# Performance work log

Hardware: AMD Instinct MI355X
Metric: run time of the kernel (lower is better)

The kernel has to match this reference:

```python
import jax, jax.numpy as jnp
import numpy as np

B, I, J, C = 1, 256, 256, 128
H, D = 4, 32          # no_heads, head_dim; c_hidden = H*D = 128
INF = 1.0e9
LN_EPS = 1e-5


def setup_inputs() -> dict:
    key = jax.random.key(0)
    ks = jax.random.split(key, 8)
    x = jax.random.normal(ks[0], (B, I, J, C), dtype=jnp.float32)
    mask = (jax.random.uniform(ks[1], (B, I, J)) > 0.1).astype(jnp.float32)
    std = 0.02
    wq = std * jax.random.normal(ks[2], (H * D, C), dtype=jnp.float32)
    wk = std * jax.random.normal(ks[3], (H * D, C), dtype=jnp.float32)
    wv = std * jax.random.normal(ks[4], (H * D, C), dtype=jnp.float32)
    wb = std * jax.random.normal(ks[5], (H, C), dtype=jnp.float32)
    wo = (std / np.sqrt(2 * H)) * jax.random.normal(ks[6], (C, H * D), dtype=jnp.float32)
    wo_b = jnp.zeros((C,), dtype=jnp.float32)
    ln_g = jnp.ones((C,), dtype=jnp.float32)
    ln_b = jnp.zeros((C,), dtype=jnp.float32)
    return {"x": x, "mask": mask, "ln_g": ln_g, "ln_b": ln_b,
            "wq": wq, "wk": wk, "wv": wv, "wb": wb, "wo": wo, "wo_b": wo_b}


def reference(x, mask, ln_g, ln_b, wq, wk, wv, wb, wo, wo_b):
    # LayerNorm over channel dim
    mu = jnp.mean(x, axis=-1, keepdims=True)
    var = jnp.mean(jnp.square(x - mu), axis=-1, keepdims=True)
    xn = (x - mu) * jax.lax.rsqrt(var + LN_EPS) * ln_g + ln_b

    # QKV projections (torch Linear: y = x @ W^T), reshape to heads
    q = (xn @ wq.T).reshape(B, I, J, H, D)
    k = (xn @ wk.T).reshape(B, I, J, H, D)
    v = (xn @ wv.T).reshape(B, I, J, H, D)

    scale = 1.0 / np.sqrt(D)
    # attention within each row i over the J dimension: [B, I, H, Jq, Jk]
    scores = jnp.einsum('biqhd,bikhd->bihqk', q, k) * scale

    # triangle bias: [B, I, J, H] -> [B, I, H, Jq, 1], broadcast over keys
    tb = jnp.einsum('bijc,hc->bijh', xn, wb)
    scores = scores + jnp.swapaxes(tb, -1, -2)[..., None]

    # mask bias: inf*(mask-1) -> [B, I, 1, Jq, 1] (as in the torch code)
    scores = scores + (INF * (mask - 1.0))[:, :, None, :, None]

    attn = jax.nn.softmax(scores, axis=-1)
    out = jnp.einsum('bihqk,bikhd->biqhd', attn, v).reshape(B, I, J, H * D)
    return out @ wo.T + wo_b
```

## Files before the change

kernel.cpp:

```cpp
#include <hip/hip_runtime.h>
#include <hip/hip_bf16.h>

typedef short bf16x8 __attribute__((ext_vector_type(8)));
typedef short bf16x4 __attribute__((ext_vector_type(4)));
typedef float f32x4  __attribute__((ext_vector_type(4)));

#define NI 256
#define NJ 256
#define NC 128
#define NH 4
#define ND 32

#define WB_OFF    0
#define WO_BF_OFF 98304
#define QG_OFF    131072
#define KG_OFF    16908288
#define VTG_OFF   37879808
#define TBM_OFF   55181312
#define OG_OFF    56229888

__device__ __forceinline__ short f2bf(float f) {
    return __builtin_bit_cast(short, __float2bfloat16(f));
}

typedef __attribute__((address_space(1))) const void gvoid_t;
typedef __attribute__((address_space(3))) void svoid_t;
__device__ __forceinline__ void load_lds16(const void* g, void* l) {
    __builtin_amdgcn_global_load_lds((gvoid_t*)g, (svoid_t*)l, 16, 0, 0);
}

__global__ __launch_bounds__(256, 8)
void k_conv(const float* __restrict__ wq, const float* __restrict__ wk,
            const float* __restrict__ wv, const float* __restrict__ wo,
            char* __restrict__ ws)
{
    const int gt = blockIdx.x * 256 + threadIdx.x;
    const int base = gt * 4;
    const float* src;
    short* dst;
    if (base < 49152) {
        const int t = base >> 14;
        src = (t == 0 ? wq : (t == 1 ? wk : wv)) + (base & 16383);
        dst = (short*)(ws + WB_OFF) + base;
    } else {
        src = wo + (base - 49152);
        dst = (short*)(ws + WO_BF_OFF) + (base - 49152);
    }
    f32x4 v = *(const f32x4*)src;
    bf16x4 o;
    #pragma unroll
    for (int r = 0; r < 4; ++r) o[r] = f2bf(v[r]);
    *(bf16x4*)dst = o;
}

__global__ __launch_bounds__(512, 4)
void k_pre(const float* __restrict__ x, const float* __restrict__ mask,
           const float* __restrict__ ln_g, const float* __restrict__ ln_b,
           const float* __restrict__ wb, char* __restrict__ ws)
{
    __shared__ char xn_s[128 * 256];

    const int tid  = threadIdx.x;
    const int lane = tid & 63;
    const int wid  = tid >> 6;
    const int g    = lane >> 4;
    const int l16  = lane & 15;
    const int b    = blockIdx.x;
    const int i    = b >> 1;
    const int half = b & 1;
    const int j0   = half * 128;

    {
        const int t  = tid >> 2;
        const int p  = tid & 3;
        const int ch = p * 32;
        const float* xr = x + ((size_t)(i * NJ) + j0 + t) * NC + ch;
        f32x4 vx[8];
        float s0 = 0.f;
        #pragma unroll
        for (int u = 0; u < 8; ++u) {
            vx[u] = *(const f32x4*)(xr + 4 * u);
            s0 += vx[u][0] + vx[u][1] + vx[u][2] + vx[u][3];
        }
        s0 += __shfl_xor(s0, 1);
        s0 += __shfl_xor(s0, 2);
        const float mu = s0 * 0.0078125f;
        float v0 = 0.f;
        #pragma unroll
        for (int u = 0; u < 8; ++u) {
            #pragma unroll
            for (int e = 0; e < 4; ++e) { float d = vx[u][e] - mu; v0 += d * d; }
        }
        v0 += __shfl_xor(v0, 1);
        v0 += __shfl_xor(v0, 2);
        const float rs = rsqrtf(v0 * 0.0078125f + 1e-5f);
        #pragma unroll
        for (int u = 0; u < 8; ++u) {
            f32x4 gg = *(const f32x4*)(ln_g + ch + 4 * u);
            f32x4 bb = *(const f32x4*)(ln_b + ch + 4 * u);
            #pragma unroll
            for (int e = 0; e < 4; ++e) vx[u][e] = (vx[u][e] - mu) * rs * gg[e] + bb[e];
        }
        float tb[4];
        #pragma unroll
        for (int h = 0; h < 4; ++h) {
            const float* wr = wb + h * NC + ch;
            float a = 0.f;
            #pragma unroll
            for (int u = 0; u < 8; ++u) {
                f32x4 w4 = *(const f32x4*)(wr + 4 * u);
                #pragma unroll
                for (int e = 0; e < 4; ++e) a += vx[u][e] * w4[e];
            }
            a += __shfl_xor(a, 1);
            a += __shfl_xor(a, 2);
            tb[h] = a;
        }
        if (p == 0) {
            const float mb = 1.0e9f * (mask[(size_t)i * NJ + j0 + t] - 1.0f);
            float* tbm = (float*)(ws + TBM_OFF);
            #pragma unroll
            for (int h = 0; h < 4; ++h)
                tbm[((size_t)(i * NH) + h) * NJ + j0 + t] = tb[h] + mb;
        }
        #pragma unroll
        for (int cc = 0; cc < 4; ++cc) {
            bf16x8 o8;
            #pragma unroll
            for (int e = 0; e < 4; ++e) {
                o8[e]     = f2bf(vx[2 * cc][e]);
                o8[4 + e] = f2bf(vx[2 * cc + 1][e]);
            }
            const int chunk = (p * 4 + cc) ^ (t & 7);
            *(bf16x8*)(xn_s + t * 256 + chunk * 16) = o8;
        }
    }
    __syncthreads();

    const f32x4 z4 = {0.f, 0.f, 0.f, 0.f};
    bf16x8 bfr[3][4];
    #pragma unroll
    for (int s = 0; s < 3; ++s) {
        const int n0 = wid * 48 + s * 16;
        const short* wr = (const short*)(ws + WB_OFF) + (size_t)(n0 + l16) * NC + g * 8;
        #pragma unroll
        for (int ks = 0; ks < 4; ++ks) bfr[s][ks] = *(const bf16x8*)(wr + ks * 32);
    }

    for (int mt = 0; mt < 8; ++mt) {
        const int row = mt * 16 + l16;
        bf16x8 af[4];
        #pragma unroll
        for (int ks = 0; ks < 4; ++ks) {
            const int chunk = (ks * 4 + g) ^ (row & 7);
            af[ks] = *(const bf16x8*)(xn_s + row * 256 + chunk * 16);
        }
        #pragma unroll
        for (int s = 0; s < 3; ++s) {
            f32x4 acc = z4;
            #pragma unroll
            for (int ks = 0; ks < 4; ++ks)
                acc = __builtin_amdgcn_mfma_f32_16x16x32_bf16(af[ks], bfr[s][ks], acc, 0, 0, 0);

            const int gr  = wid * 48 + s * 16;
            const int buf = gr >> 7;
            const int h   = (gr >> 5) & 3;
            const int dd0 = gr & 31;
            const size_t ih = (size_t)(i * NH) + h;
            const int tok = j0 + mt * 16 + g * 4;
            if (buf == 0) {
                short* qg = (short*)(ws + QG_OFF) + ih * 8192;
                #pragma unroll
                for (int r = 0; r < 4; ++r) qg[(tok + r) * 32 + dd0 + l16] = f2bf(acc[r]);
            } else if (buf == 1) {
                short* kg = (short*)(ws + KG_OFF) + ih * 10240;
                #pragma unroll
                for (int r = 0; r < 4; ++r) kg[(tok + r) * 40 + dd0 + l16] = f2bf(acc[r]);
            } else {
                short* vt = (short*)(ws + VTG_OFF) + ih * 8448;
                bf16x4 pk;
                #pragma unroll
                for (int r = 0; r < 4; ++r) pk[r] = f2bf(acc[r]);
                *(bf16x4*)(vt + (size_t)(dd0 + l16) * 264 + tok) = pk;
            }
        }
    }
}

__global__ __launch_bounds__(512, 4)
void k_attn(char* __restrict__ ws)
{
    __shared__ short kls[256][40];
    __shared__ char  vls[17408];
    __shared__ short pbuf[8][2][16][40];

    const int tid  = threadIdx.x;
    const int lane = tid & 63;
    const int wid  = tid >> 6;
    const int g    = lane >> 4;
    const int l16  = lane & 15;
    const size_t ih = blockIdx.x;
    const int i = (int)(ih >> 2);
    const int h = (int)(ih & 3);

    const short* qg  = (const short*)(ws + QG_OFF) + ih * 8192;
    const char*  kgp = ws + KG_OFF + ih * 20480;
    const char*  vtp = ws + VTG_OFF + ih * 16896;
    const float* tbm = (const float*)(ws + TBM_OFF) + ih * NJ;
    short* og = (short*)(ws + OG_OFF);

    for (int c = wid; c < 37; c += 8) {
        if (c < 20)      load_lds16(kgp + c * 1024 + lane * 16, (char*)kls + c * 1024);
        else if (c < 36) load_lds16(vtp + (c - 20) * 1024 + lane * 16, vls + (c - 20) * 1024);
        else if (lane < 32) load_lds16(vtp + 16384 + lane * 16, vls + 16384);
    }
    __syncthreads();

    const float SCALE = 0.17677669529663687f;
    const f32x4 z4 = {0.f, 0.f, 0.f, 0.f};

    #pragma unroll
    for (int qt = 0; qt < 2; ++qt) {
        const int tq = wid * 32 + qt * 16;
        f32x4 tbmb = *(const f32x4*)(tbm + tq + g * 4);

        bf16x8 qf = *(const bf16x8*)(qg + (size_t)(tq + l16) * 32 + g * 8);
        f32x4 s[16];
        #pragma unroll
        for (int kt = 0; kt < 16; ++kt) {
            bf16x8 kf = *(const bf16x8*)(&kls[kt * 16 + l16][g * 8]);
            s[kt] = __builtin_amdgcn_mfma_f32_16x16x32_bf16(qf, kf, z4, 0, 0, 0);
        }
        #pragma unroll
        for (int kt = 0; kt < 16; ++kt)
            #pragma unroll
            for (int r = 0; r < 4; ++r)
                s[kt][r] = fmaf(s[kt][r], SCALE, tbmb[r]);

        f32x4 mx = s[0];
        #pragma unroll
        for (int kt = 1; kt < 16; ++kt)
            #pragma unroll
            for (int r = 0; r < 4; ++r) mx[r] = fmaxf(mx[r], s[kt][r]);
        #pragma unroll
        for (int d = 1; d < 16; d <<= 1)
            #pragma unroll
            for (int r = 0; r < 4; ++r) mx[r] = fmaxf(mx[r], __shfl_xor(mx[r], d));

        f32x4 sum = z4;
        #pragma unroll
        for (int kt = 0; kt < 16; ++kt)
            #pragma unroll
            for (int r = 0; r < 4; ++r) { s[kt][r] = __expf(s[kt][r] - mx[r]); sum[r] += s[kt][r]; }
        #pragma unroll
        for (int d = 1; d < 16; d <<= 1)
            #pragma unroll
            for (int r = 0; r < 4; ++r) sum[r] += __shfl_xor(sum[r], d);
        f32x4 inv;
        #pragma unroll
        for (int r = 0; r < 4; ++r) inv[r] = 1.0f / sum[r];
        #pragma unroll
        for (int kt = 0; kt < 16; ++kt)
            #pragma unroll
            for (int r = 0; r < 4; ++r) s[kt][r] *= inv[r];

        f32x4 oacc0 = z4, oacc1 = z4;
        #pragma unroll
        for (int c = 0; c < 8; ++c) {
            short* pb = &pbuf[wid][c & 1][0][0];
            #pragma unroll
            for (int kk = 0; kk < 2; ++kk) {
                #pragma unroll
                for (int r = 0; r < 4; ++r)
                    pb[(g * 4 + r) * 40 + kk * 16 + l16] = f2bf(s[c * 2 + kk][r]);
            }
            bf16x8 a   = *(const bf16x8*)(pb + l16 * 40 + g * 8);
            bf16x8 vb0 = *(const bf16x8*)((const short*)(vls + (size_t)l16 * 528) + c * 32 + g * 8);
            bf16x8 vb1 = *(const bf16x8*)((const short*)(vls + (size_t)(16 + l16) * 528) + c * 32 + g * 8);
            oacc0 = __builtin_amdgcn_mfma_f32_16x16x32_bf16(a, vb0, oacc0, 0, 0, 0);
            oacc1 = __builtin_amdgcn_mfma_f32_16x16x32_bf16(a, vb1, oacc1, 0, 0, 0);
        }

        #pragma unroll
        for (int r = 0; r < 4; ++r) {
            const size_t row = (size_t)(i * NJ) + tq + g * 4 + r;
            og[row * 136 + h * 32 + l16]      = f2bf(oacc0[r]);
            og[row * 136 + h * 32 + 16 + l16] = f2bf(oacc1[r]);
        }
    }
}

__global__ __launch_bounds__(512, 4)
void k_oproj(const char* __restrict__ ws, const float* __restrict__ wo_b,
             float* __restrict__ out)
{
    __shared__ short ol[128][136];

    const int tid  = threadIdx.x;
    const int lane = tid & 63;
    const int wid  = tid >> 6;
    const int g    = lane >> 4;
    const int l16  = lane & 15;
    const size_t tok0 = (size_t)blockIdx.x * 128;

    const char* ogp = ws + OG_OFF + tok0 * 272;
    for (int c = wid; c < 34; c += 8)
        load_lds16(ogp + c * 1024 + lane * 16, (char*)ol + c * 1024);
    __syncthreads();

    const short* wrow = (const short*)(ws + WO_BF_OFF) + (size_t)(wid * 16 + l16) * NC + g * 8;
    bf16x8 bfr[4];
    #pragma unroll
    for (int ks = 0; ks < 4; ++ks) bfr[ks] = *(const bf16x8*)(wrow + ks * 32);

    const float bias = wo_b[wid * 16 + l16];
    const f32x4 z4 = {0.f, 0.f, 0.f, 0.f};

    #pragma unroll
    for (int mt = 0; mt < 8; ++mt) {
        const short* orow = &ol[mt * 16 + l16][g * 8];
        f32x4 acc = z4;
        #pragma unroll
        for (int ks = 0; ks < 4; ++ks) {
            bf16x8 av = *(const bf16x8*)(orow + ks * 32);
            acc = __builtin_amdgcn_mfma_f32_16x16x32_bf16(av, bfr[ks], acc, 0, 0, 0);
        }
        #pragma unroll
        for (int r = 0; r < 4; ++r)
            out[(tok0 + mt * 16 + g * 4 + r) * NC + wid * 16 + l16] = acc[r] + bias;
    }
}

extern "C" void kernel_launch(void* const* d_in, const int* in_sizes, int n_in,
                              void* d_out, int out_size, void* d_ws, size_t ws_size,
                              hipStream_t stream) {
    const float* x    = (const float*)d_in[0];
    const float* mask = (const float*)d_in[1];
    const float* ln_g = (const float*)d_in[2];
    const float* ln_b = (const float*)d_in[3];
    const float* wq   = (const float*)d_in[4];
    const float* wk   = (const float*)d_in[5];
    const float* wv   = (const float*)d_in[6];
    const float* wb   = (const float*)d_in[7];
    const float* wo   = (const float*)d_in[8];
    const float* wo_b = (const float*)d_in[9];
    float* out = (float*)d_out;
    char* ws   = (char*)d_ws;

    k_conv<<<dim3(64), dim3(256), 0, stream>>>(wq, wk, wv, wo, ws);
    k_pre<<<dim3(NI * 2), dim3(512), 0, stream>>>(x, mask, ln_g, ln_b, wb, ws);
    k_attn<<<dim3(NI * NH), dim3(512), 0, stream>>>(ws);
    k_oproj<<<dim3(NI * 2), dim3(512), 0, stream>>>(ws, wo_b, out);
}
```

Measured before the change: 95.58 us.

## Fuse per-head QKV projection into attention kernel, keep Q/K/V in LDS

```diff
diff --git a/kernel.cpp b/kernel.cpp
--- a/kernel.cpp
+++ b/kernel.cpp
@@ -13,11 +13,9 @@
 
 #define WB_OFF    0
 #define WO_BF_OFF 98304
-#define QG_OFF    131072
-#define KG_OFF    16908288
-#define VTG_OFF   37879808
-#define TBM_OFF   55181312
-#define OG_OFF    56229888
+#define XN_OFF    131072
+#define TBM_OFF   16908288
+#define OG_OFF    17956864
 
 __device__ __forceinline__ short f2bf(float f) {
     return __builtin_bit_cast(short, __float2bfloat16(f));
@@ -54,177 +52,149 @@
 }
 
 __global__ __launch_bounds__(512, 4)
-void k_pre(const float* __restrict__ x, const float* __restrict__ mask,
-           const float* __restrict__ ln_g, const float* __restrict__ ln_b,
-           const float* __restrict__ wb, char* __restrict__ ws)
+void k_ln(const float* __restrict__ x, const float* __restrict__ mask,
+          const float* __restrict__ ln_g, const float* __restrict__ ln_b,
+          const float* __restrict__ wb, char* __restrict__ ws)
 {
-    __shared__ char xn_s[128 * 256];
+    const int tid = threadIdx.x;
+    const int t   = tid >> 2;
+    const int p   = tid & 3;
+    const int ch  = p * 32;
+    const size_t tok = (size_t)blockIdx.x * 128 + t;
+
+    const float* xr = x + tok * NC + ch;
+    f32x4 vx[8];
+    float s0 = 0.f;
+    #pragma unroll
+    for (int u = 0; u < 8; ++u) {
+        vx[u] = *(const f32x4*)(xr + 4 * u);
+        s0 += vx[u][0] + vx[u][1] + vx[u][2] + vx[u][3];
+    }
+    s0 += __shfl_xor(s0, 1);
+    s0 += __shfl_xor(s0, 2);
+    const float mu = s0 * 0.0078125f;
+    float v0 = 0.f;
+    #pragma unroll
+    for (int u = 0; u < 8; ++u) {
+        #pragma unroll
+        for (int e = 0; e < 4; ++e) { float d = vx[u][e] - mu; v0 += d * d; }
+    }
+    v0 += __shfl_xor(v0, 1);
+    v0 += __shfl_xor(v0, 2);
+    const float rs = rsqrtf(v0 * 0.0078125f + 1e-5f);
+    #pragma unroll
+    for (int u = 0; u < 8; ++u) {
+        f32x4 gg = *(const f32x4*)(ln_g + ch + 4 * u);
+        f32x4 bb = *(const f32x4*)(ln_b + ch + 4 * u);
+        #pragma unroll
+        for (int e = 0; e < 4; ++e) vx[u][e] = (vx[u][e] - mu) * rs * gg[e] + bb[e];
+    }
+
+    float tb[4];
+    #pragma unroll
+    for (int h = 0; h < 4; ++h) {
+        const float* wr = wb + h * NC + ch;
+        float a = 0.f;
+        #pragma unroll
+        for (int u = 0; u < 8; ++u) {
+            f32x4 w4 = *(const f32x4*)(wr + 4 * u);
+            #pragma unroll
+            for (int e = 0; e < 4; ++e) a += vx[u][e] * w4[e];
+        }
+        a += __shfl_xor(a, 1);
+        a += __shfl_xor(a, 2);
+        tb[h] = a;
+    }
+    if (p == 0) {
+        const float mb = 1.0e9f * (mask[tok] - 1.0f);
+        const size_t i = tok >> 8, j = tok & 255;
+        float* tbm = (float*)(ws + TBM_OFF);
+        #pragma unroll
+        for (int h = 0; h < 4; ++h)
+            tbm[(i * NH + h) * NJ + j] = tb[h] + mb;
+    }
+
+    short* xnrow = (short*)(ws + XN_OFF) + tok * NC + ch;
+    #pragma unroll
+    for (int cc = 0; cc < 4; ++cc) {
+        bf16x8 o8;
+        #pragma unroll
+        for (int e = 0; e < 4; ++e) {
+            o8[e]     = f2bf(vx[2 * cc][e]);
+            o8[4 + e] = f2bf(vx[2 * cc + 1][e]);
+        }
+        *(bf16x8*)(xnrow + 8 * cc) = o8;
+    }
+}
+
+__global__ __launch_bounds__(512, 4)
+void k_fat(char* __restrict__ ws)
+{
+    __shared__ short kls[256][40];
+    __shared__ short vls[32][264];
+    __shared__ short pbuf[8][3][16][40];
 
     const int tid  = threadIdx.x;
     const int lane = tid & 63;
     const int wid  = tid >> 6;
     const int g    = lane >> 4;
     const int l16  = lane & 15;
-    const int b    = blockIdx.x;
-    const int i    = b >> 1;
-    const int half = b & 1;
-    const int j0   = half * 128;
-
-    {
-        const int t  = tid >> 2;
-        const int p  = tid & 3;
-        const int ch = p * 32;
-        const float* xr = x + ((size_t)(i * NJ) + j0 + t) * NC + ch;
-        f32x4 vx[8];
-        float s0 = 0.f;
-        #pragma unroll
-        for (int u = 0; u < 8; ++u) {
-            vx[u] = *(const f32x4*)(xr + 4 * u);
-            s0 += vx[u][0] + vx[u][1] + vx[u][2] + vx[u][3];
-        }
-        s0 += __shfl_xor(s0, 1);
-        s0 += __shfl_xor(s0, 2);
-        const float mu = s0 * 0.0078125f;
-        float v0 = 0.f;
-        #pragma unroll
-        for (int u = 0; u < 8; ++u) {
-            #pragma unroll
-            for (int e = 0; e < 4; ++e) { float d = vx[u][e] - mu; v0 += d * d; }
-        }
-        v0 += __shfl_xor(v0, 1);
-        v0 += __shfl_xor(v0, 2);
-        const float rs = rsqrtf(v0 * 0.0078125f + 1e-5f);
-        #pragma unroll
-        for (int u = 0; u < 8; ++u) {
-            f32x4 gg = *(const f32x4*)(ln_g + ch + 4 * u);
-            f32x4 bb = *(const f32x4*)(ln_b + ch + 4 * u);
-            #pragma unroll
-            for (int e = 0; e < 4; ++e) vx[u][e] = (vx[u][e] - mu) * rs * gg[e] + bb[e];
-        }
-        float tb[4];
-        #pragma unroll
-        for (int h = 0; h < 4; ++h) {
-            const float* wr = wb + h * NC + ch;
-            float a = 0.f;
-            #pragma unroll
-            for (int u = 0; u < 8; ++u) {
-                f32x4 w4 = *(const f32x4*)(wr + 4 * u);
+    const int ih   = blockIdx.x;
+    const int i    = ih >> 2;
+    const int h    = ih & 3;
+
+    const short* xn   = (const short*)(ws + XN_OFF) + (size_t)i * NJ * NC;
+    const short* wqkv = (const short*)(ws + WB_OFF);
+    const float* tbm  = (const float*)(ws + TBM_OFF) + (size_t)ih * NJ;
+    short* og = (short*)(ws + OG_OFF) + ((size_t)h * (NI * NJ) + (size_t)i * NJ) * ND;
+
+    const f32x4 z4 = {0.f, 0.f, 0.f, 0.f};
+
+    #pragma unroll
+    for (int tile = 0; tile < 2; ++tile) {
+        const int tq = wid * 32 + tile * 16;
+        bf16x8 af[4];
+        #pragma unroll
+        for (int ks = 0; ks < 4; ++ks)
+            af[ks] = *(const bf16x8*)(xn + (size_t)(tq + l16) * NC + ks * 32 + g * 8);
+        #pragma unroll
+        for (int op = 0; op < 3; ++op) {
+            #pragma unroll
+            for (int sub = 0; sub < 2; ++sub) {
+                const short* wrow = wqkv + (size_t)(op * 128 + h * 32 + sub * 16 + l16) * NC + g * 8;
+                f32x4 acc = z4;
                 #pragma unroll
-                for (int e = 0; e < 4; ++e) a += vx[u][e] * w4[e];
+                for (int ks = 0; ks < 4; ++ks) {
+                    bf16x8 bf = *(const bf16x8*)(wrow + ks * 32);
+                    acc = __builtin_amdgcn_mfma_f32_16x16x32_bf16(af[ks], bf, acc, 0, 0, 0);
+                }
+                if (op == 0) {
+                    #pragma unroll
+                    for (int r = 0; r < 4; ++r)
+                        pbuf[wid][tile][g * 4 + r][sub * 16 + l16] = f2bf(acc[r]);
+                } else if (op == 1) {
+                    #pragma unroll
+                    for (int r = 0; r < 4; ++r)
+                        kls[tq + g * 4 + r][sub * 16 + l16] = f2bf(acc[r]);
+                } else {
+                    bf16x4 pk;
+                    #pragma unroll
+                    for (int r = 0; r < 4; ++r) pk[r] = f2bf(acc[r]);
+                    *(bf16x4*)(&vls[sub * 16 + l16][tq + g * 4]) = pk;
+                }
             }
-            a += __shfl_xor(a, 1);
-            a += __shfl_xor(a, 2);
-            tb[h] = a;
-        }
-        if (p == 0) {
-            const float mb = 1.0e9f * (mask[(size_t)i * NJ + j0 + t] - 1.0f);
-            float* tbm = (float*)(ws + TBM_OFF);
-            #pragma unroll
-            for (int h = 0; h < 4; ++h)
-                tbm[((size_t)(i * NH) + h) * NJ + j0 + t] = tb[h] + mb;
-        }
-        #pragma unroll
-        for (int cc = 0; cc < 4; ++cc) {
-            bf16x8 o8;
-            #pragma unroll
-            for (int e = 0; e < 4; ++e) {
-                o8[e]     = f2bf(vx[2 * cc][e]);
-                o8[4 + e] = f2bf(vx[2 * cc + 1][e]);
-            }
-            const int chunk = (p * 4 + cc) ^ (t & 7);
-            *(bf16x8*)(xn_s + t * 256 + chunk * 16) = o8;
         }
     }
     __syncthreads();
 
-    const f32x4 z4 = {0.f, 0.f, 0.f, 0.f};
-    bf16x8 bfr[3][4];
-    #pragma unroll
-    for (int s = 0; s < 3; ++s) {
-        const int n0 = wid * 48 + s * 16;
-        const short* wr = (const short*)(ws + WB_OFF) + (size_t)(n0 + l16) * NC + g * 8;
-        #pragma unroll
-        for (int ks = 0; ks < 4; ++ks) bfr[s][ks] = *(const bf16x8*)(wr + ks * 32);
-    }
-
-    for (int mt = 0; mt < 8; ++mt) {
-        const int row = mt * 16 + l16;
-        bf16x8 af[4];
-        #pragma unroll
-        for (int ks = 0; ks < 4; ++ks) {
-            const int chunk = (ks * 4 + g) ^ (row & 7);
-            af[ks] = *(const bf16x8*)(xn_s + row * 256 + chunk * 16);
-        }
-        #pragma unroll
-        for (int s = 0; s < 3; ++s) {
-            f32x4 acc = z4;
-            #pragma unroll
-            for (int ks = 0; ks < 4; ++ks)
-                acc = __builtin_amdgcn_mfma_f32_16x16x32_bf16(af[ks], bfr[s][ks], acc, 0, 0, 0);
-
-            const int gr  = wid * 48 + s * 16;
-            const int buf = gr >> 7;
-            const int h   = (gr >> 5) & 3;
-            const int dd0 = gr & 31;
-            const size_t ih = (size_t)(i * NH) + h;
-            const int tok = j0 + mt * 16 + g * 4;
-            if (buf == 0) {
-                short* qg = (short*)(ws + QG_OFF) + ih * 8192;
-                #pragma unroll
-                for (int r = 0; r < 4; ++r) qg[(tok + r) * 32 + dd0 + l16] = f2bf(acc[r]);
-            } else if (buf == 1) {
-                short* kg = (short*)(ws + KG_OFF) + ih * 10240;
-                #pragma unroll
-                for (int r = 0; r < 4; ++r) kg[(tok + r) * 40 + dd0 + l16] = f2bf(acc[r]);
-            } else {
-                short* vt = (short*)(ws + VTG_OFF) + ih * 8448;
-                bf16x4 pk;
-                #pragma unroll
-                for (int r = 0; r < 4; ++r) pk[r] = f2bf(acc[r]);
-                *(bf16x4*)(vt + (size_t)(dd0 + l16) * 264 + tok) = pk;
-            }
-        }
-    }
-}
-
-__global__ __launch_bounds__(512, 4)
-void k_attn(char* __restrict__ ws)
-{
-    __shared__ short kls[256][40];
-    __shared__ char  vls[17408];
-    __shared__ short pbuf[8][2][16][40];
-
-    const int tid  = threadIdx.x;
-    const int lane = tid & 63;
-    const int wid  = tid >> 6;
-    const int g    = lane >> 4;
-    const int l16  = lane & 15;
-    const size_t ih = blockIdx.x;
-    const int i = (int)(ih >> 2);
-    const int h = (int)(ih & 3);
-
-    const short* qg  = (const short*)(ws + QG_OFF) + ih * 8192;
-    const char*  kgp = ws + KG_OFF + ih * 20480;
-    const char*  vtp = ws + VTG_OFF + ih * 16896;
-    const float* tbm = (const float*)(ws + TBM_OFF) + ih * NJ;
-    short* og = (short*)(ws + OG_OFF);
-
-    for (int c = wid; c < 37; c += 8) {
-        if (c < 20)      load_lds16(kgp + c * 1024 + lane * 16, (char*)kls + c * 1024);
-        else if (c < 36) load_lds16(vtp + (c - 20) * 1024 + lane * 16, vls + (c - 20) * 1024);
-        else if (lane < 32) load_lds16(vtp + 16384 + lane * 16, vls + 16384);
-    }
-    __syncthreads();
-
     const float SCALE = 0.17677669529663687f;
-    const f32x4 z4 = {0.f, 0.f, 0.f, 0.f};
 
     #pragma unroll
     for (int qt = 0; qt < 2; ++qt) {
         const int tq = wid * 32 + qt * 16;
         f32x4 tbmb = *(const f32x4*)(tbm + tq + g * 4);
 
-        bf16x8 qf = *(const bf16x8*)(qg + (size_t)(tq + l16) * 32 + g * 8);
+        bf16x8 qf = *(const bf16x8*)(&pbuf[wid][qt][l16][g * 8]);
         f32x4 s[16];
         #pragma unroll
         for (int kt = 0; kt < 16; ++kt) {
@@ -267,7 +237,7 @@
         f32x4 oacc0 = z4, oacc1 = z4;
         #pragma unroll
         for (int c = 0; c < 8; ++c) {
-            short* pb = &pbuf[wid][c & 1][0][0];
+            short* pb = &pbuf[wid][(c & 1) ? 0 : 2][0][0];
             #pragma unroll
             for (int kk = 0; kk < 2; ++kk) {
                 #pragma unroll
@@ -275,17 +245,17 @@
                     pb[(g * 4 + r) * 40 + kk * 16 + l16] = f2bf(s[c * 2 + kk][r]);
             }
             bf16x8 a   = *(const bf16x8*)(pb + l16 * 40 + g * 8);
-            bf16x8 vb0 = *(const bf16x8*)((const short*)(vls + (size_t)l16 * 528) + c * 32 + g * 8);
-            bf16x8 vb1 = *(const bf16x8*)((const short*)(vls + (size_t)(16 + l16) * 528) + c * 32 + g * 8);
+            bf16x8 vb0 = *(const bf16x8*)(&vls[l16][c * 32 + g * 8]);
+            bf16x8 vb1 = *(const bf16x8*)(&vls[16 + l16][c * 32 + g * 8]);
             oacc0 = __builtin_amdgcn_mfma_f32_16x16x32_bf16(a, vb0, oacc0, 0, 0, 0);
             oacc1 = __builtin_amdgcn_mfma_f32_16x16x32_bf16(a, vb1, oacc1, 0, 0, 0);
         }
 
         #pragma unroll
         for (int r = 0; r < 4; ++r) {
-            const size_t row = (size_t)(i * NJ) + tq + g * 4 + r;
-            og[row * 136 + h * 32 + l16]      = f2bf(oacc0[r]);
-            og[row * 136 + h * 32 + 16 + l16] = f2bf(oacc1[r]);
+            const int tok = tq + g * 4 + r;
+            og[(size_t)tok * ND + l16]      = f2bf(oacc0[r]);
+            og[(size_t)tok * ND + 16 + l16] = f2bf(oacc1[r]);
         }
     }
 }
@@ -294,7 +264,7 @@
 void k_oproj(const char* __restrict__ ws, const float* __restrict__ wo_b,
              float* __restrict__ out)
 {
-    __shared__ short ol[128][136];
+    __shared__ short ol[4][128][32];
 
     const int tid  = threadIdx.x;
     const int lane = tid & 63;
@@ -303,9 +273,12 @@
     const int l16  = lane & 15;
     const size_t tok0 = (size_t)blockIdx.x * 128;
 
-    const char* ogp = ws + OG_OFF + tok0 * 272;
-    for (int c = wid; c < 34; c += 8)
-        load_lds16(ogp + c * 1024 + lane * 16, (char*)ol + c * 1024);
+    const short* ogb = (const short*)(ws + OG_OFF);
+    for (int c = wid; c < 32; c += 8) {
+        const int hh = c >> 3, cc = c & 7;
+        const char* src = (const char*)(ogb + ((size_t)hh * (NI * NJ) + tok0) * ND) + cc * 1024 + lane * 16;
+        load_lds16(src, (char*)ol + c * 1024);
+    }
     __syncthreads();
 
     const short* wrow = (const short*)(ws + WO_BF_OFF) + (size_t)(wid * 16 + l16) * NC + g * 8;
@@ -318,11 +291,10 @@
 
     #pragma unroll
     for (int mt = 0; mt < 8; ++mt) {
-        const short* orow = &ol[mt * 16 + l16][g * 8];
         f32x4 acc = z4;
         #pragma unroll
         for (int ks = 0; ks < 4; ++ks) {
-            bf16x8 av = *(const bf16x8*)(orow + ks * 32);
+            bf16x8 av = *(const bf16x8*)(&ol[ks][mt * 16 + l16][g * 8]);
             acc = __builtin_amdgcn_mfma_f32_16x16x32_bf16(av, bfr[ks], acc, 0, 0, 0);
         }
         #pragma unroll
@@ -347,8 +319,8 @@
     float* out = (float*)d_out;
     char* ws   = (char*)d_ws;
 
-    k_conv<<<dim3(64), dim3(256), 0, stream>>>(wq, wk, wv, wo, ws);
-    k_pre<<<dim3(NI * 2), dim3(512), 0, stream>>>(x, mask, ln_g, ln_b, wb, ws);
-    k_attn<<<dim3(NI * NH), dim3(512), 0, stream>>>(ws);
-    k_oproj<<<dim3(NI * 2), dim3(512), 0, stream>>>(ws, wo_b, out);
-}
+    k_conv <<<dim3(64),     dim3(256), 0, stream>>>(wq, wk, wv, wo, ws);
+    k_ln   <<<dim3(512),    dim3(512), 0, stream>>>(x, mask, ln_g, ln_b, wb, ws);
+    k_fat  <<<dim3(NI * NH), dim3(512), 0, stream>>>(ws);
+    k_oproj<<<dim3(512),    dim3(512), 0, stream>>>(ws, wo_b, out);
+}
```

Result: slower. 107.1 us (+12.1%).
